# Kernel optimization log

Hardware: AMD Instinct MI355X
Metric: run time of the kernel (lower is better)

Reference implementation:

```python
import jax, jax.numpy as jnp
import numpy as np

NUM_HEADS = 16
HEAD_DIM = 64


def setup_inputs() -> dict:
    key = jax.random.key(0)
    ks = jax.random.split(key, 12)
    B, T, C = 2, 2048, 1024
    H, D = NUM_HEADS, HEAD_DIM
    s_in = 1.0 / np.sqrt(C)
    return {
        "x": jax.random.normal(ks[0], (B, T, C), dtype=jnp.float32),
        "mask": jnp.ones((B, 1, 1, T), dtype=bool),
        "plasticity_scalar": jax.random.uniform(ks[1], (B, 1), dtype=jnp.float32),
        "wq": jax.random.normal(ks[2], (C, H * D), dtype=jnp.float32) * s_in,
        "bq": jnp.zeros((H * D,), dtype=jnp.float32),
        "wk": jax.random.normal(ks[3], (C, H * D), dtype=jnp.float32) * s_in,
        "bk": jnp.zeros((H * D,), dtype=jnp.float32),
        "wv": jax.random.normal(ks[4], (C, H * D), dtype=jnp.float32) * s_in,
        "bv": jnp.zeros((H * D,), dtype=jnp.float32),
        "wmod": jax.random.normal(ks[5], (1, H * 2), dtype=jnp.float32),
        "bmod": jnp.zeros((H * 2,), dtype=jnp.float32),
        "wo": jax.random.normal(ks[6], (H * D, C), dtype=jnp.float32) * (1.0 / np.sqrt(H * D)),
        "bo": jnp.zeros((C,), dtype=jnp.float32),
    }


def reference(x, mask, plasticity_scalar, wq, bq, wk, bk, wv, bv, wmod, bmod, wo, bo):
    B, T, C = x.shape
    H, D = NUM_HEADS, HEAD_DIM
    q = (x @ wq + bq).reshape(B, T, H, D)
    k = (x @ wk + bk).reshape(B, T, H, D)
    v = (x @ wv + bv).reshape(B, T, H, D)
    # scores[b,h,s,t] = sum_d q[b,t,h,d] * k[b,s,h,d]  (as in original einsum)
    scores = jnp.einsum('bthd,bshd->bhst', q, k) * (1.0 / jnp.sqrt(jnp.float32(D)))
    modulator = (plasticity_scalar @ wmod + bmod).reshape(B, H, 2)
    temp_scale = 1.0 + jax.nn.softplus(modulator[:, :, 0])  # [B, H]
    scores = scores / temp_scale[:, :, None, None]
    diag_bias = modulator[:, :, 1][:, :, None, None] * jnp.eye(T, dtype=scores.dtype)[None, None, :, :]
    scores = scores + diag_bias
    scores = jnp.where(mask, scores, -1000000000.0)
    attn = jax.nn.softmax(scores, axis=-1)  # softmax over t (last axis), as in original
    o = jnp.einsum('bhst,bshd->bthd', attn, v).reshape(B, T, H * D)
    out = o @ wo + bo
    return (out, temp_scale)
```

## Files before the change

### kernel.cpp

```cpp
#include <hip/hip_runtime.h>

#define B_ 2
#define T_ 2048
#define C_ 1024
#define H_ 16
#define HD_ 1024
#define QLD 3072
#define LOG2E 1.4426950408889634f

typedef unsigned short u16;
typedef short bf16x8 __attribute__((ext_vector_type(8)));
typedef float f32x4 __attribute__((ext_vector_type(4)));
typedef float f32x16 __attribute__((ext_vector_type(16)));
typedef u16 u16x8 __attribute__((ext_vector_type(8)));

__device__ __forceinline__ u16 f2bf(float f) {
  unsigned u = __float_as_uint(f);
  u += 0x7FFFu + ((u >> 16) & 1u);
  return (u16)(u >> 16);
}
__device__ __forceinline__ float bf2f(u16 h) { return __uint_as_float(((unsigned)h) << 16); }

__device__ __forceinline__ unsigned cvt_pk_bf16(float lo, float hi) {
  unsigned r;
  asm("v_cvt_pk_bf16_f32 %0, %1, %2" : "=v"(r) : "v"(lo), "v"(hi));
  return r;
}
__device__ __forceinline__ float fexp2(float x) {
  float r;
  asm("v_exp_f32 %0, %1" : "=v"(r) : "v"(x));
  return r;
}

__device__ __forceinline__ void gload16(const void* g, void* l) {
  __builtin_amdgcn_global_load_lds(
      (const __attribute__((address_space(1))) unsigned int*)g,
      (__attribute__((address_space(3))) unsigned int*)l, 16, 0, 0);
}

#define VM_WAIT(n) asm volatile("s_waitcnt vmcnt(" #n ")" ::: "memory")
#define BAR() asm volatile("s_barrier" ::: "memory")

#define MFMA16(a, b, c) __builtin_amdgcn_mfma_f32_16x16x32_bf16((a), (b), (c), 0, 0, 0)
#define MFMA32(a, b, c) __builtin_amdgcn_mfma_f32_32x32x16_bf16((a), (b), (c), 0, 0, 0)

__global__ void prep_kernel(const float* ps, const float* wmod, const float* bmod,
                            float* out_tail, float* scale_buf, float* diag_buf) {
  int t = threadIdx.x;
  if (t < B_ * H_) {
    int b = t >> 4, h = t & 15;
    float p = ps[b];
    float m0 = p * wmod[2 * h] + bmod[2 * h];
    float m1 = p * wmod[2 * h + 1] + bmod[2 * h + 1];
    float sp = (m0 > 20.f) ? m0 : log1pf(expf(m0));
    float temp = 1.f + sp;
    out_tail[t] = temp;
    scale_buf[t] = LOG2E / (8.f * temp);
    diag_buf[t] = m1 * LOG2E;
  }
}

__global__ void convert_x(const float* __restrict__ x, u16* __restrict__ xb) {
  int i = blockIdx.x * 256 + threadIdx.x;
  float4 v = ((const float4*)x)[i];
  ushort4 o;
  o.x = f2bf(v.x); o.y = f2bf(v.y); o.z = f2bf(v.z); o.w = f2bf(v.w);
  ((ushort4*)xb)[i] = o;
}

__global__ void convert_w_t(const float* wq, const float* wk, const float* wv,
                            const float* wo, u16* qkvT, u16* woT) {
  int z = blockIdx.z;
  const float* w = (z == 0) ? wq : (z == 1) ? wk : (z == 2) ? wv : wo;
  u16* wt = (z == 3) ? woT : qkvT + (size_t)z * 1024 * 1024;
  __shared__ float tile[64][65];
  int k0 = blockIdx.x * 64, n0 = blockIdx.y * 64;
  int tid = threadIdx.x;
  int r = tid >> 4, c = (tid & 15) * 4;
#pragma unroll
  for (int i = 0; i < 4; i++) {
    float4 v = *(const float4*)(w + (size_t)(k0 + r + i * 16) * 1024 + n0 + c);
    tile[r + i * 16][c] = v.x; tile[r + i * 16][c + 1] = v.y;
    tile[r + i * 16][c + 2] = v.z; tile[r + i * 16][c + 3] = v.w;
  }
  __syncthreads();
#pragma unroll
  for (int i = 0; i < 4; i++) {
    int rn = r + i * 16;
    ushort4 o;
    o.x = f2bf(tile[c][rn]); o.y = f2bf(tile[c + 1][rn]);
    o.z = f2bf(tile[c + 2][rn]); o.w = f2bf(tile[c + 3][rn]);
    *(ushort4*)(wt + (size_t)(n0 + rn) * 1024 + k0 + c) = o;
  }
}

__global__ __launch_bounds__(256) void gemm_qkv(const u16* __restrict__ A, const u16* __restrict__ BT,
                                                const float* __restrict__ bq, const float* __restrict__ bk,
                                                const float* __restrict__ bv,
                                                const float* __restrict__ scale_buf,
                                                u16* __restrict__ Cout) {
  __shared__ u16 As[128 * 32];
  __shared__ u16 Bs[128 * 32];
  int m0 = blockIdx.x * 128, n0 = blockIdx.y * 128;
  int tid = threadIdx.x;
  int w = tid >> 6, l = tid & 63;
  int wr = w >> 1, wc = w & 1;
  int lrow = l & 15, kb = l >> 4;
  int r = tid >> 2, c = tid & 3;
  f32x4 acc[4][4] = {};
  for (int k0 = 0; k0 < C_; k0 += 32) {
#pragma unroll
    for (int j = 0; j < 2; j++) {
      gload16(A + (size_t)(m0 + r + j * 64) * C_ + k0 + c * 8, (char*)As + (r + j * 64) * 64 + c * 16);
      gload16(BT + (size_t)(n0 + r + j * 64) * C_ + k0 + c * 8, (char*)Bs + (r + j * 64) * 64 + c * 16);
    }
    __syncthreads();
    bf16x8 af[4], bfv[4];
#pragma unroll
    for (int mi = 0; mi < 4; mi++) af[mi] = *(const bf16x8*)(As + (wr * 64 + mi * 16 + lrow) * 32 + kb * 8);
#pragma unroll
    for (int ni = 0; ni < 4; ni++) bfv[ni] = *(const bf16x8*)(Bs + (wc * 64 + ni * 16 + lrow) * 32 + kb * 8);
#pragma unroll
    for (int mi = 0; mi < 4; mi++)
#pragma unroll
      for (int ni = 0; ni < 4; ni++) acc[mi][ni] = MFMA16(af[mi], bfv[ni], acc[mi][ni]);
    __syncthreads();
  }
  int bb = m0 >> 11;
#pragma unroll
  for (int mi = 0; mi < 4; mi++)
#pragma unroll
    for (int ni = 0; ni < 4; ni++) {
      int gcol = n0 + wc * 64 + ni * 16 + lrow;
      int sect = gcol >> 10;
      const float* bp = (sect == 0) ? bq : (sect == 1) ? bk : bv;
      float bvf = bp[gcol & 1023];
      float fac = (sect == 0) ? scale_buf[bb * 16 + ((gcol >> 6) & 15)] : 1.f;
#pragma unroll
      for (int rr = 0; rr < 4; rr++) {
        int grow = m0 + wr * 64 + mi * 16 + kb * 4 + rr;
        Cout[(size_t)grow * QLD + gcol] = f2bf((acc[mi][ni][rr] + bvf) * fac);
      }
    }
}

__global__ __launch_bounds__(256) void gemm_bt_f32(const u16* __restrict__ A, const u16* __restrict__ BT,
                                                   const float* __restrict__ bias, float* __restrict__ Cout,
                                                   int N, int K) {
  __shared__ u16 As[128 * 32];
  __shared__ u16 Bs[128 * 32];
  int m0 = blockIdx.x * 128, n0 = blockIdx.y * 128;
  int tid = threadIdx.x;
  int w = tid >> 6, l = tid & 63;
  int wr = w >> 1, wc = w & 1;
  int lrow = l & 15, kb = l >> 4;
  int r = tid >> 2, c = tid & 3;
  f32x4 acc[4][4] = {};
  for (int k0 = 0; k0 < K; k0 += 32) {
#pragma unroll
    for (int j = 0; j < 2; j++) {
      gload16(A + (size_t)(m0 + r + j * 64) * K + k0 + c * 8, (char*)As + (r + j * 64) * 64 + c * 16);
      gload16(BT + (size_t)(n0 + r + j * 64) * K + k0 + c * 8, (char*)Bs + (r + j * 64) * 64 + c * 16);
    }
    __syncthreads();
    bf16x8 af[4], bfv[4];
#pragma unroll
    for (int mi = 0; mi < 4; mi++) af[mi] = *(const bf16x8*)(As + (wr * 64 + mi * 16 + lrow) * 32 + kb * 8);
#pragma unroll
    for (int ni = 0; ni < 4; ni++) bfv[ni] = *(const bf16x8*)(Bs + (wc * 64 + ni * 16 + lrow) * 32 + kb * 8);
#pragma unroll
    for (int mi = 0; mi < 4; mi++)
#pragma unroll
      for (int ni = 0; ni < 4; ni++) acc[mi][ni] = MFMA16(af[mi], bfv[ni], acc[mi][ni]);
    __syncthreads();
  }
#pragma unroll
  for (int mi = 0; mi < 4; mi++)
#pragma unroll
    for (int ni = 0; ni < 4; ni++) {
      int gcol = n0 + wc * 64 + ni * 16 + lrow;
      float bvf = bias[gcol];
#pragma unroll
      for (int rr = 0; rr < 4; rr++) {
        int grow = m0 + wr * 64 + mi * 16 + kb * 4 + rr;
        Cout[(size_t)grow * N + gcol] = acc[mi][ni][rr] + bvf;
      }
    }
}

__global__ __launch_bounds__(512) void attn_pass1(const u16* __restrict__ q, const u16* __restrict__ k,
                                                  const int* __restrict__ mask,
                                                  const float* __restrict__ diag_buf,
                                                  float* __restrict__ l_part) {
  __shared__ u16 Qs[4][64 * 64];
  int bh = blockIdx.x, b = bh >> 4, h = bh & 15;
  int s0b = blockIdx.y * 256;
  int half = blockIdx.z;
  int tid = threadIdx.x, w = tid >> 6, l = tid & 63;
  int lane31 = l & 31, hi = l >> 5;
  float diagb = diag_buf[bh];
  int s_wb = s0b + w * 32;
  int s_g = s_wb + lane31;
  bool dhit = (((l >> 2) & 1) == hi);
  int dreg = (l & 3) + 4 * ((l >> 3) & 3);
  int sr = tid >> 3, slotL = tid & 7;
  int slotG = slotL ^ (sr & 7);
  bf16x8 kf[4];
#pragma unroll
  for (int ks = 0; ks < 4; ks++)
    kf[ks] = *(const bf16x8*)(k + (size_t)(b * T_ + s_g) * QLD + h * 64 + ks * 16 + hi * 8);

  int tbase = half * 1024;
#define STAGE_Q(buf, t0g)                                                     \
  gload16(q + (size_t)(b * T_ + (t0g) + sr) * QLD + h * 64 + slotG * 8,       \
          (char*)Qs[buf] + sr * 128 + slotL * 16)

#define P1_COMPUTE(IT)                                                        \
  {                                                                           \
    const u16* Qc = Qs[(IT) & 3];                                             \
    int t0 = tbase + (IT) * 64;                                               \
    _Pragma("unroll") for (int sub = 0; sub < 2; sub++) {                     \
      int tloc = sub * 32;                                                    \
      f32x16 sacc = {};                                                       \
      _Pragma("unroll") for (int ks = 0; ks < 4; ks++) {                      \
        int row = tloc + lane31;                                              \
        int slot = (ks * 2 + hi) ^ (row & 7);                                 \
        bf16x8 qa = *(const bf16x8*)(Qc + row * 64 + slot * 8);               \
        sacc = MFMA32(qa, kf[ks], sacc);                                      \
      }                                                                       \
      if (t0 + tloc == s_wb) {                                                \
        _Pragma("unroll") for (int r = 0; r < 16; r++)                        \
            sacc[r] += (dhit && r == dreg) ? diagb : 0.f;                     \
      }                                                                       \
      int mv = mask[b * T_ + t0 + tloc + lane31];                             \
      bool allset = (~__ballot(mv != 0)) == 0ull;                             \
      if (allset) {                                                           \
        _Pragma("unroll") for (int r = 0; r < 16; r++) lsum += fexp2(sacc[r]); \
      } else {                                                                \
        float mvf = mv ? 1.f : 0.f;                                           \
        _Pragma("unroll") for (int r = 0; r < 16; r++) {                      \
          float mp = __shfl(mvf, (r & 3) + 8 * (r >> 2) + 4 * hi, 64);        \
          lsum += mp * fexp2(sacc[r]);                                        \
        }                                                                     \
      }                                                                       \
    }                                                                         \
  }

  float lsum = 0.f;
  STAGE_Q(0, tbase);
  STAGE_Q(1, tbase + 64);
  for (int it = 0; it < 14; it++) {
    STAGE_Q((it + 2) & 3, tbase + (it + 2) * 64);
    VM_WAIT(2);
    BAR();
    P1_COMPUTE(it);
  }
  VM_WAIT(1);
  BAR();
  P1_COMPUTE(14);
  VM_WAIT(0);
  BAR();
  P1_COMPUTE(15);
  float total = lsum + __shfl_xor(lsum, 32, 64);
  if (hi == 0) l_part[half * (32 * 2048) + bh * 2048 + s_g] = total;
#undef STAGE_Q
#undef P1_COMPUTE
}

__global__ void scale_transpose_v(const u16* __restrict__ qkv, const float* __restrict__ l_part,
                                  u16* __restrict__ vT) {
  __shared__ float tile[64][65];
  int st0 = blockIdx.x * 64;
  int hd0 = blockIdx.y * 64;
  int tid = threadIdx.x;
  int r = tid >> 4, c4 = (tid & 15) * 4;
#pragma unroll
  for (int i = 0; i < 4; i++) {
    int row = r + i * 16;
    ushort4 hh = *(const ushort4*)(qkv + (size_t)(st0 + row) * QLD + 2048 + hd0 + c4);
    tile[row][c4] = bf2f(hh.x); tile[row][c4 + 1] = bf2f(hh.y);
    tile[row][c4 + 2] = bf2f(hh.z); tile[row][c4 + 3] = bf2f(hh.w);
  }
  __syncthreads();
  int b = st0 >> 11, sbase = st0 & 2047, h = hd0 >> 6, bh = b * 16 + h;
#pragma unroll
  for (int i = 0; i < 4; i++) {
    int dl = r + i * 16;
    ushort4 o4;
#pragma unroll
    for (int j = 0; j < 4; j++) {
      int s = sbase + c4 + j;
      float il = 1.f / (l_part[bh * 2048 + s] + l_part[32 * 2048 + bh * 2048 + s]);
      ((u16*)&o4)[j] = f2bf(tile[c4 + j][dl] * il);
    }
    *(ushort4*)(vT + (size_t)(bh * 64 + dl) * T_ + sbase + c4) = o4;
  }
}

__global__ __launch_bounds__(512) void attn_pass2(const u16* __restrict__ q, const u16* __restrict__ k,
                                                  const u16* __restrict__ vT,
                                                  const int* __restrict__ mask,
                                                  const float* __restrict__ diag_buf,
                                                  u16* __restrict__ obp) {
  __shared__ u16 Ks[4][64 * 64];
  __shared__ u16 Vs[4][64 * 64];
  int bh = blockIdx.x, b = bh >> 4, h = bh & 15;
  int t0 = blockIdx.y * 256;
  int shalf = blockIdx.z;
  int s_start = shalf * 1024;
  u16* op = obp + (size_t)shalf * 4096 * 1024;
  int tid = threadIdx.x, w = tid >> 6, l = tid & 63;
  int lane31 = l & 31, hi = l >> 5;
  float diagb = diag_buf[bh];
  int t_wb = t0 + w * 32;
  int t_g = t_wb + lane31;
  bool dhit = (((l >> 2) & 1) == hi);
  int dreg = (l & 3) + 4 * ((l >> 3) & 3);
  int sr = tid >> 3, slotL = tid & 7;
  int slotG = slotL ^ (sr & 7);
  bf16x8 qf[4];
#pragma unroll
  for (int ks = 0; ks < 4; ks++)
    qf[ks] = *(const bf16x8*)(q + (size_t)(b * T_ + t_g) * QLD + h * 64 + ks * 16 + hi * 8);
  int mv = mask[b * T_ + t_g];
  float tmf = mv ? 1.f : 0.f;
  bool allset = (~__ballot(mv != 0)) == 0ull;
  f32x16 oacc0 = {}, oacc1 = {};

#define STAGE_KV(buf, s0g)                                                    \
  {                                                                           \
    gload16(k + (size_t)(b * T_ + (s0g) + sr) * QLD + h * 64 + slotG * 8,     \
            (char*)Ks[buf] + sr * 128 + slotL * 16);                          \
    gload16(vT + (size_t)(bh * 64 + sr) * T_ + (s0g) + slotG * 8,             \
            (char*)Vs[buf] + sr * 128 + slotL * 16);                          \
  }

#define P2_COMPUTE(SI)                                                        \
  {                                                                           \
    const u16* Kc = Ks[(SI) & 3];                                             \
    const u16* Vc = Vs[(SI) & 3];                                             \
    int s0 = s_start + (SI) * 64;                                             \
    _Pragma("unroll") for (int sub = 0; sub < 2; sub++) {                     \
      int ss = sub * 32;                                                      \
      f32x16 sacc = {};                                                       \
      _Pragma("unroll") for (int ks = 0; ks < 4; ks++) {                      \
        int row = ss + lane31;                                                \
        int slot = (ks * 2 + hi) ^ (row & 7);                                 \
        bf16x8 kfr = *(const bf16x8*)(Kc + row * 64 + slot * 8);              \
        sacc = MFMA32(kfr, qf[ks], sacc);                                     \
      }                                                                       \
      if (s0 + ss == t_wb) {                                                  \
        _Pragma("unroll") for (int r = 0; r < 16; r++)                        \
            sacc[r] += (dhit && r == dreg) ? diagb : 0.f;                     \
      }                                                                       \
      float p[16];                                                            \
      _Pragma("unroll") for (int r = 0; r < 16; r++) p[r] = fexp2(sacc[r]);   \
      if (!allset) {                                                          \
        _Pragma("unroll") for (int r = 0; r < 16; r++) p[r] *= tmf;           \
      }                                                                       \
      unsigned pk[8];                                                         \
      _Pragma("unroll") for (int i = 0; i < 8; i++)                           \
          pk[i] = cvt_pk_bf16(p[2 * i], p[2 * i + 1]);                        \
      _Pragma("unroll") for (int ps = 0; ps < 2; ps++) {                      \
        unsigned a0 = pk[4 * ps + 0], a2 = pk[4 * ps + 2];                    \
        unsigned a1 = pk[4 * ps + 1], a3 = pk[4 * ps + 3];                    \
        asm("v_permlane32_swap_b32 %0, %1" : "+v"(a0), "+v"(a2));             \
        asm("v_permlane32_swap_b32 %0, %1" : "+v"(a1), "+v"(a3));             \
        union { unsigned u[4]; bf16x8 v; } fr;                                \
        fr.u[0] = a0; fr.u[1] = a1; fr.u[2] = a2; fr.u[3] = a3;               \
        _Pragma("unroll") for (int dh = 0; dh < 2; dh++) {                    \
          int row = dh * 32 + lane31;                                         \
          int slot = ((ss >> 3) + ps * 2 + hi) ^ (row & 7);                   \
          bf16x8 vfr = *(const bf16x8*)(Vc + row * 64 + slot * 8);            \
          if (dh == 0) oacc0 = MFMA32(fr.v, vfr, oacc0);                      \
          else oacc1 = MFMA32(fr.v, vfr, oacc1);                              \
        }                                                                     \
      }                                                                       \
    }                                                                         \
  }

  STAGE_KV(0, s_start);
  STAGE_KV(1, s_start + 64);
  for (int si = 0; si < 14; si++) {
    STAGE_KV((si + 2) & 3, s_start + (si + 2) * 64);
    VM_WAIT(4);
    BAR();
    P2_COMPUTE(si);
  }
  VM_WAIT(2);
  BAR();
  P2_COMPUTE(14);
  VM_WAIT(0);
  BAR();
  P2_COMPUTE(15);
#pragma unroll
  for (int r = 0; r < 16; r++) {
    int t_out = t0 + w * 32 + ((r & 3) + 8 * (r >> 2) + 4 * hi);
    size_t base = (size_t)(b * T_ + t_out) * HD_ + h * 64;
    op[base + lane31] = f2bf(oacc0[r]);
    op[base + 32 + lane31] = f2bf(oacc1[r]);
  }
#undef STAGE_KV
#undef P2_COMPUTE
}

__global__ void merge_o(const u16* __restrict__ p0, const u16* __restrict__ p1,
                        u16* __restrict__ ob) {
  int i = blockIdx.x * 256 + threadIdx.x;
  u16x8 a = ((const u16x8*)p0)[i];
  u16x8 b = ((const u16x8*)p1)[i];
  u16x8 o;
#pragma unroll
  for (int j = 0; j < 8; j++) o[j] = f2bf(bf2f(a[j]) + bf2f(b[j]));
  ((u16x8*)ob)[i] = o;
}

extern "C" void kernel_launch(void* const* d_in, const int* in_sizes, int n_in,
                              void* d_out, int out_size, void* d_ws, size_t ws_size,
                              hipStream_t stream) {
  const float* x = (const float*)d_in[0];
  const int* mask = (const int*)d_in[1];
  const float* ps = (const float*)d_in[2];
  const float* wq = (const float*)d_in[3];
  const float* bq = (const float*)d_in[4];
  const float* wk = (const float*)d_in[5];
  const float* bk = (const float*)d_in[6];
  const float* wv = (const float*)d_in[7];
  const float* bv = (const float*)d_in[8];
  const float* wmod = (const float*)d_in[9];
  const float* bmod = (const float*)d_in[10];
  const float* wo = (const float*)d_in[11];
  const float* bo = (const float*)d_in[12];
  float* out = (float*)d_out;

  const size_t MB = 1ull << 20;
  char* ws = (char*)d_ws;
  u16* xb    = (u16*)(ws + 0 * MB);
  u16* qkvT  = (u16*)(ws + 8 * MB);
  u16* woT   = (u16*)(ws + 14 * MB);
  u16* qkv   = (u16*)(ws + 16 * MB);
  u16* vT    = (u16*)(ws + 40 * MB);
  u16* ob    = (u16*)(ws + 48 * MB);
  float* l_part    = (float*)(ws + 56 * MB);
  float* scale_buf = (float*)(ws + 56 * MB + 0x80000);
  float* diag_buf  = (float*)(ws + 56 * MB + 0x80100);
  u16* obp   = (u16*)(ws + 64 * MB);

  prep_kernel<<<1, 64, 0, stream>>>(ps, wmod, bmod, out + (size_t)B_ * T_ * C_, scale_buf, diag_buf);
  convert_x<<<4096, 256, 0, stream>>>(x, xb);
  convert_w_t<<<dim3(16, 16, 4), 256, 0, stream>>>(wq, wk, wv, wo, qkvT, woT);
  gemm_qkv<<<dim3(32, 24), 256, 0, stream>>>(xb, qkvT, bq, bk, bv, scale_buf, qkv);
  attn_pass1<<<dim3(32, 8, 2), 512, 0, stream>>>(qkv, qkv + 1024, mask, diag_buf, l_part);
  scale_transpose_v<<<dim3(64, 16), 256, 0, stream>>>(qkv, l_part, vT);
  attn_pass2<<<dim3(32, 8, 2), 512, 0, stream>>>(qkv, qkv + 1024, vT, mask, diag_buf, obp);
  merge_o<<<2048, 256, 0, stream>>>(obp, obp + (size_t)4096 * 1024, ob);
  gemm_bt_f32<<<dim3(32, 8), 256, 0, stream>>>(ob, woT, bo, out, C_, C_);
}
```

Baseline: 156.2 us.

## Pipeline GEMM global-to-LDS loads with a four-stage shared-memory ring

Both the QKV projection and output projection GEMMs now use a 4-buffer LDS ring, prefetching two K-tiles ahead with vmcnt waits and one barrier per iteration instead of two. This hides global load latency behind MFMA work. The cost is more LDS per block (64KB), which may lower occupancy. The output GEMM also hardcodes N and K to C_.

```diff
diff --git a/kernel.cpp b/kernel.cpp
--- a/kernel.cpp
+++ b/kernel.cpp
@@ -99,8 +99,8 @@
                                                 const float* __restrict__ bv,
                                                 const float* __restrict__ scale_buf,
                                                 u16* __restrict__ Cout) {
-  __shared__ u16 As[128 * 32];
-  __shared__ u16 Bs[128 * 32];
+  __shared__ u16 As[4][128 * 32];
+  __shared__ u16 Bs[4][128 * 32];
   int m0 = blockIdx.x * 128, n0 = blockIdx.y * 128;
   int tid = threadIdx.x;
   int w = tid >> 6, l = tid & 63;
@@ -108,24 +108,48 @@
   int lrow = l & 15, kb = l >> 4;
   int r = tid >> 2, c = tid & 3;
   f32x4 acc[4][4] = {};
-  for (int k0 = 0; k0 < C_; k0 += 32) {
-#pragma unroll
-    for (int j = 0; j < 2; j++) {
-      gload16(A + (size_t)(m0 + r + j * 64) * C_ + k0 + c * 8, (char*)As + (r + j * 64) * 64 + c * 16);
-      gload16(BT + (size_t)(n0 + r + j * 64) * C_ + k0 + c * 8, (char*)Bs + (r + j * 64) * 64 + c * 16);
-    }
-    __syncthreads();
-    bf16x8 af[4], bfv[4];
-#pragma unroll
-    for (int mi = 0; mi < 4; mi++) af[mi] = *(const bf16x8*)(As + (wr * 64 + mi * 16 + lrow) * 32 + kb * 8);
-#pragma unroll
-    for (int ni = 0; ni < 4; ni++) bfv[ni] = *(const bf16x8*)(Bs + (wc * 64 + ni * 16 + lrow) * 32 + kb * 8);
-#pragma unroll
-    for (int mi = 0; mi < 4; mi++)
-#pragma unroll
-      for (int ni = 0; ni < 4; ni++) acc[mi][ni] = MFMA16(af[mi], bfv[ni], acc[mi][ni]);
-    __syncthreads();
-  }
+
+#define GQ_STAGE(buf, k0g)                                                                  \
+  {                                                                                         \
+    _Pragma("unroll") for (int j = 0; j < 2; j++) {                                         \
+      gload16(A + (size_t)(m0 + r + j * 64) * C_ + (k0g) + c * 8,                           \
+              (char*)As[buf] + (r + j * 64) * 64 + c * 16);                                 \
+      gload16(BT + (size_t)(n0 + r + j * 64) * C_ + (k0g) + c * 8,                          \
+              (char*)Bs[buf] + (r + j * 64) * 64 + c * 16);                                 \
+    }                                                                                       \
+  }
+
+#define GQ_COMPUTE(IT)                                                                      \
+  {                                                                                         \
+    const u16* Ac = As[(IT) & 3];                                                           \
+    const u16* Bc = Bs[(IT) & 3];                                                           \
+    bf16x8 af[4], bfv[4];                                                                   \
+    _Pragma("unroll") for (int mi = 0; mi < 4; mi++)                                        \
+        af[mi] = *(const bf16x8*)(Ac + (wr * 64 + mi * 16 + lrow) * 32 + kb * 8);           \
+    _Pragma("unroll") for (int ni = 0; ni < 4; ni++)                                        \
+        bfv[ni] = *(const bf16x8*)(Bc + (wc * 64 + ni * 16 + lrow) * 32 + kb * 8);          \
+    _Pragma("unroll") for (int mi = 0; mi < 4; mi++)                                        \
+        _Pragma("unroll") for (int ni = 0; ni < 4; ni++)                                    \
+            acc[mi][ni] = MFMA16(af[mi], bfv[ni], acc[mi][ni]);                             \
+  }
+
+  GQ_STAGE(0, 0);
+  GQ_STAGE(1, 32);
+  for (int i = 0; i < 30; i++) {
+    GQ_STAGE((i + 2) & 3, (i + 2) * 32);
+    VM_WAIT(8);
+    BAR();
+    GQ_COMPUTE(i);
+  }
+  VM_WAIT(4);
+  BAR();
+  GQ_COMPUTE(30);
+  VM_WAIT(0);
+  BAR();
+  GQ_COMPUTE(31);
+#undef GQ_STAGE
+#undef GQ_COMPUTE
+
   int bb = m0 >> 11;
 #pragma unroll
   for (int mi = 0; mi < 4; mi++)
@@ -145,10 +169,10 @@
 }
 
 __global__ __launch_bounds__(256) void gemm_bt_f32(const u16* __restrict__ A, const u16* __restrict__ BT,
-                                                   const float* __restrict__ bias, float* __restrict__ Cout,
-                                                   int N, int K) {
-  __shared__ u16 As[128 * 32];
-  __shared__ u16 Bs[128 * 32];
+                                                   const float* __restrict__ bias,
+                                                   float* __restrict__ Cout) {
+  __shared__ u16 As[4][128 * 32];
+  __shared__ u16 Bs[4][128 * 32];
   int m0 = blockIdx.x * 128, n0 = blockIdx.y * 128;
   int tid = threadIdx.x;
   int w = tid >> 6, l = tid & 63;
@@ -156,24 +180,48 @@
   int lrow = l & 15, kb = l >> 4;
   int r = tid >> 2, c = tid & 3;
   f32x4 acc[4][4] = {};
-  for (int k0 = 0; k0 < K; k0 += 32) {
-#pragma unroll
-    for (int j = 0; j < 2; j++) {
-      gload16(A + (size_t)(m0 + r + j * 64) * K + k0 + c * 8, (char*)As + (r + j * 64) * 64 + c * 16);
-      gload16(BT + (size_t)(n0 + r + j * 64) * K + k0 + c * 8, (char*)Bs + (r + j * 64) * 64 + c * 16);
-    }
-    __syncthreads();
-    bf16x8 af[4], bfv[4];
-#pragma unroll
-    for (int mi = 0; mi < 4; mi++) af[mi] = *(const bf16x8*)(As + (wr * 64 + mi * 16 + lrow) * 32 + kb * 8);
-#pragma unroll
-    for (int ni = 0; ni < 4; ni++) bfv[ni] = *(const bf16x8*)(Bs + (wc * 64 + ni * 16 + lrow) * 32 + kb * 8);
-#pragma unroll
-    for (int mi = 0; mi < 4; mi++)
-#pragma unroll
-      for (int ni = 0; ni < 4; ni++) acc[mi][ni] = MFMA16(af[mi], bfv[ni], acc[mi][ni]);
-    __syncthreads();
-  }
+
+#define GB_STAGE(buf, k0g)                                                                  \
+  {                                                                                         \
+    _Pragma("unroll") for (int j = 0; j < 2; j++) {                                         \
+      gload16(A + (size_t)(m0 + r + j * 64) * C_ + (k0g) + c * 8,                           \
+              (char*)As[buf] + (r + j * 64) * 64 + c * 16);                                 \
+      gload16(BT + (size_t)(n0 + r + j * 64) * C_ + (k0g) + c * 8,                          \
+              (char*)Bs[buf] + (r + j * 64) * 64 + c * 16);                                 \
+    }                                                                                       \
+  }
+
+#define GB_COMPUTE(IT)                                                                      \
+  {                                                                                         \
+    const u16* Ac = As[(IT) & 3];                                                           \
+    const u16* Bc = Bs[(IT) & 3];                                                           \
+    bf16x8 af[4], bfv[4];                                                                   \
+    _Pragma("unroll") for (int mi = 0; mi < 4; mi++)                                        \
+        af[mi] = *(const bf16x8*)(Ac + (wr * 64 + mi * 16 + lrow) * 32 + kb * 8);           \
+    _Pragma("unroll") for (int ni = 0; ni < 4; ni++)                                        \
+        bfv[ni] = *(const bf16x8*)(Bc + (wc * 64 + ni * 16 + lrow) * 32 + kb * 8);          \
+    _Pragma("unroll") for (int mi = 0; mi < 4; mi++)                                        \
+        _Pragma("unroll") for (int ni = 0; ni < 4; ni++)                                    \
+            acc[mi][ni] = MFMA16(af[mi], bfv[ni], acc[mi][ni]);                             \
+  }
+
+  GB_STAGE(0, 0);
+  GB_STAGE(1, 32);
+  for (int i = 0; i < 30; i++) {
+    GB_STAGE((i + 2) & 3, (i + 2) * 32);
+    VM_WAIT(8);
+    BAR();
+    GB_COMPUTE(i);
+  }
+  VM_WAIT(4);
+  BAR();
+  GB_COMPUTE(30);
+  VM_WAIT(0);
+  BAR();
+  GB_COMPUTE(31);
+#undef GB_STAGE
+#undef GB_COMPUTE
+
 #pragma unroll
   for (int mi = 0; mi < 4; mi++)
 #pragma unroll
@@ -183,7 +231,7 @@
 #pragma unroll
       for (int rr = 0; rr < 4; rr++) {
         int grow = m0 + wr * 64 + mi * 16 + kb * 4 + rr;
-        Cout[(size_t)grow * N + gcol] = acc[mi][ni][rr] + bvf;
+        Cout[(size_t)grow * C_ + gcol] = acc[mi][ni][rr] + bvf;
       }
     }
 }
@@ -454,5 +502,5 @@
   scale_transpose_v<<<dim3(64, 16), 256, 0, stream>>>(qkv, l_part, vT);
   attn_pass2<<<dim3(32, 8, 2), 512, 0, stream>>>(qkv, qkv + 1024, vT, mask, diag_buf, obp);
   merge_o<<<2048, 256, 0, stream>>>(obp, obp + (size_t)4096 * 1024, ob);
-  gemm_bt_f32<<<dim3(32, 8), 256, 0, stream>>>(ob, woT, bo, out, C_, C_);
-}
+  gemm_bt_f32<<<dim3(32, 8), 256, 0, stream>>>(ob, woT, bo, out);
+}
```

New measurement: 157.6 us. Within noise of the previous version (+0.9%).
